# Optimization experiments

Hardware: AMD Instinct MI355X
Metric: run time of the kernel (lower is better)

Reference implementation:

```python
import jax, jax.numpy as jnp
import numpy as np

B = 128          # graphs
N = 512          # nodes per graph
NT = B * N       # total nodes = 65536
E = NT * 16      # total edges = 1048576
IN = 64
H = 128
OUT = 2
L = 4            # num_layers
RATIO = 0.8


def setup_inputs() -> dict:
    key = jax.random.key(0)
    ks = jax.random.split(key, 20)

    def w(k, shape, fan_in):
        return jax.random.normal(k, shape, jnp.float32) / np.sqrt(fan_in)

    x = jax.random.normal(ks[0], (NT, IN), jnp.float32)
    edge_index = jax.random.randint(ks[1], (2, E), 0, NT, dtype=jnp.int32)
    batch = (jnp.arange(NT) // N).astype(jnp.int32)  # equal-size graphs

    return {
        "x": x,
        "edge_index": edge_index,
        "batch": batch,
        # conv1: GraphConv(IN, H, aggr='mean') -> lin_rel (w/ bias) + lin_root (no bias)
        "W1_rel": w(ks[2], (IN, H), IN),
        "W1_root": w(ks[3], (IN, H), IN),
        "b1": jnp.zeros((H,), jnp.float32),
        # convs[0..2]: GraphConv(H, H, aggr='mean'), stacked
        "Wc_rel": w(ks[4], (L - 1, H, H), H),
        "Wc_root": w(ks[5], (L - 1, H, H), H),
        "bc": jnp.zeros((L - 1, H), jnp.float32),
        # SAGPooling score GNN: GraphConv(H, 1) with default aggr='add'
        "pw_rel": w(ks[6], (H,), H),
        "pw_root": w(ks[7], (H,), H),
        "pb": jnp.zeros((1,), jnp.float32),
        # MLP head
        "lin1_W": w(ks[8], (L * H, H), L * H),
        "lin1_b": jnp.zeros((H,), jnp.float32),
        "lin2_W": w(ks[9], (H, OUT), H),
        "lin2_b": jnp.zeros((OUT,), jnp.float32),
    }


def _graph_conv_mean(x, src, dst, emask, W_rel, W_root, b, n):
    # PyG GraphConv: lin_rel(mean_{j->i} x_j) + lin_root(x_i); masked edges excluded.
    msg = x[src] * emask[:, None]                                  # [E, D] gather
    s = jax.ops.segment_sum(msg, dst, num_segments=n)              # [n, D] scatter-add
    cnt = jax.ops.segment_sum(emask, dst, num_segments=n)          # [n]
    agg = s / jnp.maximum(cnt, 1.0)[:, None]                       # zero for isolated nodes
    return agg @ W_rel + x @ W_root + b


def reference(x, edge_index, batch, W1_rel, W1_root, b1, Wc_rel, Wc_root, bc,
              pw_rel, pw_root, pb, lin1_W, lin1_b, lin2_W, lin2_b):
    src = edge_index[0]
    dst = edge_index[1]
    emask = jnp.ones((E,), jnp.float32)
    n = NT
    npg = N  # nodes per graph (all graphs equal size)

    h = jax.nn.relu(_graph_conv_mean(x, src, dst, emask, W1_rel, W1_root, b1, n))
    xs = [h.reshape(B, npg, H).mean(axis=1)]  # global_mean_pool

    for i in range(L - 1):
        h = jax.nn.relu(_graph_conv_mean(h, src, dst, emask, Wc_rel[i], Wc_root[i], bc[i], n))
        xs.append(h.reshape(B, npg, H).mean(axis=1))
        if i % 2 == 0 and i < L - 2:
            # ---- SAGPooling: score via GraphConv(H,1) with add aggregation ----
            smsg = jax.ops.segment_sum(h[src] * emask[:, None], dst, num_segments=n)
            score = smsg @ pw_rel + h @ pw_root + pb[0]            # [n]
            k = int(np.ceil(RATIO * npg))
            topv, topi = jax.lax.top_k(score.reshape(B, npg), k)   # per-graph top-k
            perm = (jnp.arange(B)[:, None] * npg + topi).reshape(-1)  # global kept ids
            h = h[perm] * jnp.tanh(topv.reshape(-1))[:, None]
            # remap edges; edges touching dropped nodes get masked out
            node_map = jnp.full((n,), -1, jnp.int32).at[perm].set(
                jnp.arange(B * k, dtype=jnp.int32))
            ns, nd = node_map[src], node_map[dst]
            keep = ((ns >= 0) & (nd >= 0)).astype(jnp.float32)
            emask = emask * keep
            src = jnp.where(ns >= 0, ns, 0)
            dst = jnp.where(nd >= 0, nd, 0)
            n = B * k
            npg = k

    xcat = jnp.concatenate(xs, axis=-1)                            # JumpingKnowledge 'cat'
    out = jax.nn.relu(xcat @ lin1_W + lin1_b)
    # dropout is identity in eval mode
    out = out @ lin2_W + lin2_b
    return jax.nn.log_softmax(out, axis=-1)
```

## Files before the change

### kernel.cpp

```cpp
#include <hip/hip_runtime.h>
#include <math.h>

#define NT 65536
#define EE 1048576
#define NB 128
#define KK 410
#define HH 128

typedef short bf16x8 __attribute__((ext_vector_type(8)));
typedef float f32x4 __attribute__((ext_vector_type(4)));

__device__ unsigned short g_xb[(size_t)NT * 64];
__device__ unsigned short g_hb1[(size_t)NT * HH];
__device__ unsigned short g_hb2[(size_t)NT * HH];
__device__ unsigned short g_wt1[128 * 128];
__device__ unsigned short g_wtc[3 * 128 * 256];
__device__ unsigned short g_csr1u[EE];
__device__ unsigned short g_keptu[NT];
__device__ unsigned int g_ebuck[EE];
__device__ int g_bcnt[128];
__device__ int g_bcur[128];
__device__ float g_trel[NT];
__device__ float g_troot[NT];
__device__ float g_gatef[NT];
__device__ float g_kinv[NT];
__device__ float g_xc4[4 * NB * 4 * 128];
__device__ int g_rows1[NT + 1];

__device__ __forceinline__ unsigned short* ubuf(int id) {
    switch (id) {
        case 0: return g_xb;
        case 1: return g_hb1;
        case 2: return g_hb2;
        case 3: return g_wt1;
        case 4: return g_wtc;
    }
    return g_xb;
}

__device__ __forceinline__ float b2f(unsigned short u) {
    union { unsigned int i; float f; } v;
    v.i = ((unsigned int)u) << 16;
    return v.f;
}
__device__ __forceinline__ unsigned short f2b(float f) {
    unsigned int x = __float_as_uint(f);
    unsigned int r = x + 0x7fffu + ((x >> 16) & 1u);
    return (unsigned short)(r >> 16);
}
__device__ __forceinline__ bf16x8 scale8(bf16x8 a, float g) {
    bf16x8 r;
#pragma unroll
    for (int i = 0; i < 8; i++) {
        unsigned short u = (unsigned short)a[i];
        r[i] = (short)f2b(b2f(u) * g);
    }
    return r;
}

__global__ __launch_bounds__(256) void k_prep(const float* __restrict__ x,
                                              const float* __restrict__ W1r,
                                              const float* __restrict__ W1o,
                                              const float* __restrict__ Wcr,
                                              const float* __restrict__ Wco,
                                              const int* __restrict__ dst) {
    if (blockIdx.x < 4544) {
        int tid = blockIdx.x * 256 + threadIdx.x;
        if (tid < 1048576) {
            float4 v = *(const float4*)&x[(size_t)tid * 4];
            unsigned int lo = (unsigned int)f2b(v.x) | ((unsigned int)f2b(v.y) << 16);
            unsigned int hi = (unsigned int)f2b(v.z) | ((unsigned int)f2b(v.w) << 16);
            *(uint2*)&g_xb[(size_t)tid * 4] = make_uint2(lo, hi);
        } else if (tid < 1048576 + 16384) {
            int r = tid - 1048576;
            int k = r & 127, n = r >> 7;
            float v = (k < 64) ? W1r[k * 128 + n] : W1o[(k - 64) * 128 + n];
            g_wt1[n * 128 + k] = f2b(v);
        } else {
            int r = tid - (1048576 + 16384);
            int l = r >> 15;
            int k = r & 255, n = (r >> 8) & 127;
            float v = (k < 128) ? Wcr[l * 16384 + k * 128 + n]
                                : Wco[l * 16384 + (k - 128) * 128 + n];
            g_wtc[l * 32768 + n * 256 + k] = f2b(v);
        }
    } else {
        __shared__ int h[128];
        if (threadIdx.x < 128) h[threadIdx.x] = 0;
        __syncthreads();
        int e0 = ((blockIdx.x - 4544) * 256 + threadIdx.x) * 4;
        int4 d = *(const int4*)&dst[e0];
        atomicAdd(&h[d.x >> 9], 1);
        atomicAdd(&h[d.y >> 9], 1);
        atomicAdd(&h[d.z >> 9], 1);
        atomicAdd(&h[d.w >> 9], 1);
        __syncthreads();
        if (threadIdx.x < 128 && h[threadIdx.x]) atomicAdd(&g_bcnt[threadIdx.x], h[threadIdx.x]);
    }
}

__global__ __launch_bounds__(256) void k_bscatter(const int* __restrict__ src,
                                                  const int* __restrict__ dst) {
    __shared__ int h[128];
    __shared__ int base[128];
    __shared__ int sc[128];
    __shared__ int vv[128];
    int t = threadIdx.x;
    if (t < 128) { vv[t] = g_bcnt[t]; sc[t] = vv[t]; h[t] = 0; }
    __syncthreads();
    for (int off = 1; off < 128; off <<= 1) {
        int u = (t >= off && t < 128) ? sc[t - off] : 0;
        __syncthreads();
        if (t < 128) sc[t] += u;
        __syncthreads();
    }
    int e0 = (blockIdx.x * 256 + t) * 4;
    int4 s = *(const int4*)&src[e0];
    int4 d = *(const int4*)&dst[e0];
    int b0 = d.x >> 9, b1 = d.y >> 9, b2 = d.z >> 9, b3 = d.w >> 9;
    atomicAdd(&h[b0], 1);
    atomicAdd(&h[b1], 1);
    atomicAdd(&h[b2], 1);
    atomicAdd(&h[b3], 1);
    __syncthreads();
    if (t < 128) {
        int c = h[t];
        base[t] = (sc[t] - vv[t]) + (c ? atomicAdd(&g_bcur[t], c) : 0);
        h[t] = 0;
    }
    __syncthreads();
    int r0 = atomicAdd(&h[b0], 1);
    g_ebuck[base[b0] + r0] = ((unsigned int)(d.x & 511) << 16) | (unsigned int)s.x;
    int r1 = atomicAdd(&h[b1], 1);
    g_ebuck[base[b1] + r1] = ((unsigned int)(d.y & 511) << 16) | (unsigned int)s.y;
    int r2 = atomicAdd(&h[b2], 1);
    g_ebuck[base[b2] + r2] = ((unsigned int)(d.z & 511) << 16) | (unsigned int)s.z;
    int r3 = atomicAdd(&h[b3], 1);
    g_ebuck[base[b3] + r3] = ((unsigned int)(d.w & 511) << 16) | (unsigned int)s.w;
}

__global__ __launch_bounds__(512) void k_bcsr() {
    __shared__ int hist[512];
    __shared__ int offs[512];
    __shared__ int cur[512];
    __shared__ int sc[128];
    int g = blockIdx.x, t = threadIdx.x;
    if (t < 128) sc[t] = g_bcnt[t];
    hist[t] = 0;
    cur[t] = 0;
    __syncthreads();
    for (int off = 1; off < 128; off <<= 1) {
        int u = (t >= off && t < 128) ? sc[t - off] : 0;
        __syncthreads();
        if (t < 128) sc[t] += u;
        __syncthreads();
    }
    int b0 = sc[g] - g_bcnt[g];
    int b1 = sc[g];
    for (int e = b0 + t; e < b1; e += 512) {
        unsigned int p = g_ebuck[e];
        atomicAdd(&hist[p >> 16], 1);
    }
    __syncthreads();
    int v = hist[t];
    offs[t] = v;
    __syncthreads();
    for (int off = 1; off < 512; off <<= 1) {
        int u = (t >= off) ? offs[t - off] : 0;
        __syncthreads();
        offs[t] += u;
        __syncthreads();
    }
    int excl = offs[t] - v;
    g_rows1[g * 512 + t] = b0 + excl;
    if (t == 511) g_rows1[g * 512 + 512] = b0 + excl + v;
    __syncthreads();
    offs[t] = excl;
    __syncthreads();
    for (int e = b0 + t; e < b1; e += 512) {
        unsigned int p = g_ebuck[e];
        int dl = p >> 16;
        int r = atomicAdd(&cur[dl], 1);
        g_csr1u[b0 + offs[dl] + r] = (unsigned short)(p & 0xFFFFu);
    }
}

template <int KA, int KB, int KC, int GATED, int MASKED, int DOTS, int BGATE>
__global__ __launch_bounds__(512) void k_conv(int hId, int bId, int wId, int wOfs,
                                              const float* __restrict__ bias, int outId,
                                              int sec,
                                              const float* __restrict__ pwr,
                                              const float* __restrict__ pwt) {
    constexpr int STR = KA + 8;
    __shared__ unsigned short lds_a[128 * STR];
    __shared__ float s[128];
    const unsigned short* h = ubuf(hId);
    const unsigned short* Bp = ubuf(bId);
    const unsigned short* Wt = ubuf(wId) + wOfs;
    unsigned short* out = ubuf(outId);
    int rowbase = blockIdx.x * 128;

    {
        constexpr int TPN = KA / 8;
        constexpr int RPP = 512 / TPN;
        int local = threadIdx.x / TPN;
        int t = threadIdx.x % TPN;
        const unsigned short* ht = h + t * 8;
#pragma unroll 1
        for (int pass = 0; pass < 128 / RPP; pass++) {
            int rl = pass * RPP + local;
            int node = rowbase + rl;
            int r0 = g_rows1[node], r1 = g_rows1[node + 1];
            float kinv_pre = (KC == 2) ? g_kinv[node] : 0.f;
            float acc[8];
#pragma unroll
            for (int i = 0; i < 8; i++) acc[i] = 0.f;
            int kc = 0;
#define ACCV(v, gf)                                              \
    acc[0] += gf * b2f((unsigned short)(v.x & 0xffff));          \
    acc[1] += gf * b2f((unsigned short)(v.x >> 16));             \
    acc[2] += gf * b2f((unsigned short)(v.y & 0xffff));          \
    acc[3] += gf * b2f((unsigned short)(v.y >> 16));             \
    acc[4] += gf * b2f((unsigned short)(v.z & 0xffff));          \
    acc[5] += gf * b2f((unsigned short)(v.z >> 16));             \
    acc[6] += gf * b2f((unsigned short)(v.w & 0xffff));          \
    acc[7] += gf * b2f((unsigned short)(v.w >> 16));
            int e = r0;
            for (; e + 4 <= r1; e += 4) {
                int i0 = g_csr1u[e], i1 = g_csr1u[e + 1];
                int i2 = g_csr1u[e + 2], i3 = g_csr1u[e + 3];
                uint4 v0 = *(const uint4*)&ht[(size_t)i0 * KA];
                uint4 v1 = *(const uint4*)&ht[(size_t)i1 * KA];
                uint4 v2 = *(const uint4*)&ht[(size_t)i2 * KA];
                uint4 v3 = *(const uint4*)&ht[(size_t)i3 * KA];
                float g0 = GATED ? g_gatef[i0] : 1.0f;
                float g1 = GATED ? g_gatef[i1] : 1.0f;
                float g2 = GATED ? g_gatef[i2] : 1.0f;
                float g3 = GATED ? g_gatef[i3] : 1.0f;
                if (KC == 1)
                    kc += (int)g_keptu[i0] + (int)g_keptu[i1]
                        + (int)g_keptu[i2] + (int)g_keptu[i3];
                ACCV(v0, g0) ACCV(v1, g1) ACCV(v2, g2) ACCV(v3, g3)
            }
            for (; e < r1; e++) {
                int i0 = g_csr1u[e];
                uint4 v0 = *(const uint4*)&ht[(size_t)i0 * KA];
                float g0 = GATED ? g_gatef[i0] : 1.0f;
                if (KC == 1) kc += (int)g_keptu[i0];
                ACCV(v0, g0)
            }
#undef ACCV
            float inv;
            if (KC == 0) {
                int c = r1 - r0;
                inv = 1.0f / (float)(c > 0 ? c : 1);
            } else if (KC == 1) {
                inv = 1.0f / (float)(kc > 0 ? kc : 1);
                if (t == 0) g_kinv[node] = inv;
            } else {
                inv = kinv_pre;
            }
            uint4 o;
            o.x = (unsigned int)f2b(acc[0] * inv) | ((unsigned int)f2b(acc[1] * inv) << 16);
            o.y = (unsigned int)f2b(acc[2] * inv) | ((unsigned int)f2b(acc[3] * inv) << 16);
            o.z = (unsigned int)f2b(acc[4] * inv) | ((unsigned int)f2b(acc[5] * inv) << 16);
            o.w = (unsigned int)f2b(acc[6] * inv) | ((unsigned int)f2b(acc[7] * inv) << 16);
            *(uint4*)&lds_a[rl * STR + t * 8] = o;
        }
    }
    __syncthreads();

    const int K = KA + KB;
    int lane = threadIdx.x & 63;
    int w = threadIdx.x >> 6;
    int n16 = lane & 15, quad = lane >> 4;
    int rowloc = w * 16;
    int rowg = rowbase + rowloc;
    int g = blockIdx.x >> 2, qb = blockIdx.x & 3;
    float ga0 = BGATE ? g_gatef[rowg + n16] : 1.0f;
    f32x4 acc[8];
#pragma unroll
    for (int ct = 0; ct < 8; ct++)
#pragma unroll
        for (int i = 0; i < 4; i++) acc[ct][i] = 0.f;

#pragma unroll
    for (int ks = 0; ks < K / 32; ks++) {
        int k0 = ks * 32;
        bf16x8 a0;
        if (k0 < KA) {
            a0 = *(const bf16x8*)&lds_a[(rowloc + n16) * STR + k0 + quad * 8];
        } else {
            int kk = k0 - KA;
            a0 = *(const bf16x8*)&Bp[(size_t)(rowg + n16) * KB + kk + quad * 8];
            if (BGATE) a0 = scale8(a0, ga0);
        }
#pragma unroll
        for (int ct = 0; ct < 8; ct++) {
            bf16x8 b = *(const bf16x8*)&Wt[(size_t)(ct * 16 + n16) * K + k0 + quad * 8];
            acc[ct] = __builtin_amdgcn_mfma_f32_16x16x32_bf16(a0, b, acc[ct], 0, 0, 0);
        }
    }

    if (threadIdx.x < 128) s[threadIdx.x] = 0.f;
    {
        float m[4];
#pragma unroll
        for (int i = 0; i < 4; i++) {
            int r = rowg + quad * 4 + i;
            m[i] = (!MASKED || g_keptu[r]) ? 1.0f : 0.0f;
        }
#pragma unroll
        for (int ct = 0; ct < 8; ct++) {
            int c = ct * 16 + n16;
            float bv = bias[c];
#pragma unroll
            for (int i = 0; i < 4; i++) {
                int r = rowg + quad * 4 + i;
                float v = fmaxf(acc[ct][i] + bv, 0.f) * m[i];
                acc[ct][i] = v;
                out[(size_t)r * 128 + c] = f2b(v);
            }
        }
    }
    __syncthreads();

#pragma unroll
    for (int ct = 0; ct < 8; ct++) {
        float p = acc[ct][0] + acc[ct][1] + acc[ct][2] + acc[ct][3];
        p += __shfl_xor(p, 16);
        p += __shfl_xor(p, 32);
        if (quad == 0) atomicAdd(&s[ct * 16 + n16], p);
    }

    if (DOTS) {
        float pr[8], pt[8];
#pragma unroll
        for (int ct = 0; ct < 8; ct++) {
            pr[ct] = pwr[ct * 16 + n16];
            pt[ct] = pwt[ct * 16 + n16];
        }
#pragma unroll
        for (int i = 0; i < 4; i++) {
            float dr = 0.f, dt = 0.f;
#pragma unroll
            for (int ct = 0; ct < 8; ct++) {
                dr += acc[ct][i] * pr[ct];
                dt += acc[ct][i] * pt[ct];
            }
            dr += __shfl_xor(dr, 1); dt += __shfl_xor(dt, 1);
            dr += __shfl_xor(dr, 2); dt += __shfl_xor(dt, 2);
            dr += __shfl_xor(dr, 4); dt += __shfl_xor(dt, 4);
            dr += __shfl_xor(dr, 8); dt += __shfl_xor(dt, 8);
            if (n16 == 0) {
                int r = rowg + quad * 4 + i;
                g_trel[r] = dr;
                g_troot[r] = dt;
            }
        }
    }
    __syncthreads();
    if (threadIdx.x < 128)
        g_xc4[((sec * NB + g) * 4 + qb) * 128 + threadIdx.x] = s[threadIdx.x];
}

__global__ __launch_bounds__(256) void k_topk(const float* __restrict__ pb) {
    __shared__ float sv[512];
    __shared__ int si[512];
    int g = blockIdx.x, t = threadIdx.x;
    if (t == 0) { g_bcnt[g] = 0; g_bcur[g] = 0; }
    float pbv = pb[0];
    for (int l = t; l < 512; l += 256) {
        int node = g * 512 + l;
        int r0 = g_rows1[node], r1 = g_rows1[node + 1];
        float s = 0.f;
        int e = r0;
        for (; e + 4 <= r1; e += 4) {
            float s0 = g_trel[g_csr1u[e]];
            float s1 = g_trel[g_csr1u[e + 1]];
            float s2 = g_trel[g_csr1u[e + 2]];
            float s3 = g_trel[g_csr1u[e + 3]];
            s += (s0 + s1) + (s2 + s3);
        }
        for (; e < r1; e++) s += g_trel[g_csr1u[e]];
        sv[l] = s + g_troot[node] + pbv;
        si[l] = l;
    }
    __syncthreads();
    for (int k = 2; k <= 512; k <<= 1) {
        for (int j = k >> 1; j > 0; j >>= 1) {
            for (int i = t; i < 512; i += 256) {
                int p = i ^ j;
                if (p > i) {
                    float va = sv[i], vb = sv[p];
                    int ia = si[i], ib = si[p];
                    bool aFirst = (va > vb) || (va == vb && ia < ib);
                    bool up = ((i & k) == 0);
                    if (up != aFirst) { sv[i] = vb; sv[p] = va; si[i] = ib; si[p] = ia; }
                }
            }
            __syncthreads();
        }
    }
    for (int r = t; r < 512; r += 256) {
        int old = g * 512 + si[r];
        if (r < KK) {
            g_gatef[old] = tanhf(sv[r]);
            g_keptu[old] = 1;
        } else {
            g_gatef[old] = 0.f;
            g_keptu[old] = 0;
        }
    }
}

__global__ __launch_bounds__(128) void k_head(const float* __restrict__ W1, const float* __restrict__ b1,
                                              const float* __restrict__ W2, const float* __restrict__ b2,
                                              float* __restrict__ out) {
    __shared__ float xr[512];
    __shared__ float r0[128], r1[128];
    int g = blockIdx.x, t = threadIdx.x;
    for (int i = t; i < 512; i += 128) {
        int sec = i >> 7, c = i & 127;
        const float* p = &g_xc4[((sec * NB + g) * 4) * 128 + c];
        float v = p[0] + p[128] + p[256] + p[384];
        float inv = (sec < 2) ? (1.0f / 512.0f) : (1.0f / 410.0f);
        xr[i] = v * inv;
    }
    __syncthreads();
    float acc = b1[t];
    for (int k = 0; k < 512; k++) acc += xr[k] * W1[k * 128 + t];
    acc = fmaxf(acc, 0.f);
    r0[t] = acc * W2[t * 2 + 0];
    r1[t] = acc * W2[t * 2 + 1];
    __syncthreads();
    for (int off = 64; off > 0; off >>= 1) {
        if (t < off) { r0[t] += r0[t + off]; r1[t] += r1[t + off]; }
        __syncthreads();
    }
    if (t == 0) {
        float z0 = r0[0] + b2[0], z1 = r1[0] + b2[1];
        float m = fmaxf(z0, z1);
        float l = m + logf(expf(z0 - m) + expf(z1 - m));
        out[g * 2 + 0] = z0 - l;
        out[g * 2 + 1] = z1 - l;
    }
}

extern "C" void kernel_launch(void* const* d_in, const int* in_sizes, int n_in,
                              void* d_out, int out_size, void* d_ws, size_t ws_size,
                              hipStream_t stream) {
    const float* x = (const float*)d_in[0];
    const int* ei = (const int*)d_in[1];
    const int* src = ei;
    const int* dst = ei + EE;
    const float* W1r = (const float*)d_in[3];
    const float* W1o = (const float*)d_in[4];
    const float* b1 = (const float*)d_in[5];
    const float* Wcr = (const float*)d_in[6];
    const float* Wco = (const float*)d_in[7];
    const float* bc = (const float*)d_in[8];
    const float* pwr = (const float*)d_in[9];
    const float* pwt = (const float*)d_in[10];
    const float* pb = (const float*)d_in[11];
    const float* l1W = (const float*)d_in[12];
    const float* l1b = (const float*)d_in[13];
    const float* l2W = (const float*)d_in[14];
    const float* l2b = (const float*)d_in[15];
    float* out = (float*)d_out;

    k_prep<<<5568, 256, 0, stream>>>(x, W1r, W1o, Wcr, Wco, dst);

    k_bscatter<<<1024, 256, 0, stream>>>(src, dst);
    k_bcsr<<<128, 512, 0, stream>>>();

    k_conv<64, 64, 0, 0, 0, 0, 0><<<512, 512, 0, stream>>>(0, 0, 3, 0, b1, 1, 0, pwr, pwt);

    k_conv<128, 128, 0, 0, 0, 1, 0><<<512, 512, 0, stream>>>(1, 1, 4, 0, bc, 2, 1, pwr, pwt);

    k_topk<<<NB, 256, 0, stream>>>(pb);

    k_conv<128, 128, 1, 1, 1, 0, 1><<<512, 512, 0, stream>>>(2, 2, 4, 32768, bc + 128, 1, 2, pwr, pwt);

    k_conv<128, 128, 2, 0, 1, 0, 0><<<512, 512, 0, stream>>>(1, 1, 4, 65536, bc + 256, 2, 3, pwr, pwt);

    k_head<<<NB, 128, 0, stream>>>(l1W, l1b, l2W, l2b, out);
}
```

Baseline: 500.8 us.

## Aggregate neighbors directly into MFMA A-fragments in registers, drop LDS staging

The conv kernel's gather-mean aggregation now has each lane accumulate the exact bf16x8 slice it will feed to the MFMA as its A operand. Aggregated rows therefore stay in registers instead of being written to LDS and read back after a barrier. Blocks shrink to 256 threads covering 64 rows, so the grid doubles and the pooled-sum partials buffer grows from 4 to 8 slots per graph, with the head summing 8. Each lane now issues 16 B gathers per channel chunk for its node, which raises register pressure and changes the memory-level parallelism of the gather.

```diff
diff --git a/kernel.cpp b/kernel.cpp
--- a/kernel.cpp
+++ b/kernel.cpp
@@ -24,7 +24,7 @@
 __device__ float g_troot[NT];
 __device__ float g_gatef[NT];
 __device__ float g_kinv[NT];
-__device__ float g_xc4[4 * NB * 4 * 128];
+__device__ float g_xc8[4 * NB * 8 * 128];
 __device__ int g_rows1[NT + 1];
 
 __device__ __forceinline__ unsigned short* ubuf(int id) {
@@ -186,123 +186,114 @@
 }
 
 template <int KA, int KB, int KC, int GATED, int MASKED, int DOTS, int BGATE>
-__global__ __launch_bounds__(512) void k_conv(int hId, int bId, int wId, int wOfs,
-                                              const float* __restrict__ bias, int outId,
-                                              int sec,
-                                              const float* __restrict__ pwr,
-                                              const float* __restrict__ pwt) {
-    constexpr int STR = KA + 8;
-    __shared__ unsigned short lds_a[128 * STR];
-    __shared__ float s[128];
+__global__ __launch_bounds__(256, 4) void k_conv(int hId, int bId, int wId, int wOfs,
+                                                 const float* __restrict__ bias, int outId,
+                                                 int sec,
+                                                 const float* __restrict__ pwr,
+                                                 const float* __restrict__ pwt) {
+    constexpr int NCHA = KA / 32;
+    const int K = KA + KB;
     const unsigned short* h = ubuf(hId);
     const unsigned short* Bp = ubuf(bId);
     const unsigned short* Wt = ubuf(wId) + wOfs;
     unsigned short* out = ubuf(outId);
-    int rowbase = blockIdx.x * 128;
-
-    {
-        constexpr int TPN = KA / 8;
-        constexpr int RPP = 512 / TPN;
-        int local = threadIdx.x / TPN;
-        int t = threadIdx.x % TPN;
-        const unsigned short* ht = h + t * 8;
-#pragma unroll 1
-        for (int pass = 0; pass < 128 / RPP; pass++) {
-            int rl = pass * RPP + local;
-            int node = rowbase + rl;
-            int r0 = g_rows1[node], r1 = g_rows1[node + 1];
-            float kinv_pre = (KC == 2) ? g_kinv[node] : 0.f;
-            float acc[8];
-#pragma unroll
-            for (int i = 0; i < 8; i++) acc[i] = 0.f;
-            int kc = 0;
-#define ACCV(v, gf)                                              \
-    acc[0] += gf * b2f((unsigned short)(v.x & 0xffff));          \
-    acc[1] += gf * b2f((unsigned short)(v.x >> 16));             \
-    acc[2] += gf * b2f((unsigned short)(v.y & 0xffff));          \
-    acc[3] += gf * b2f((unsigned short)(v.y >> 16));             \
-    acc[4] += gf * b2f((unsigned short)(v.z & 0xffff));          \
-    acc[5] += gf * b2f((unsigned short)(v.z >> 16));             \
-    acc[6] += gf * b2f((unsigned short)(v.w & 0xffff));          \
-    acc[7] += gf * b2f((unsigned short)(v.w >> 16));
-            int e = r0;
-            for (; e + 4 <= r1; e += 4) {
-                int i0 = g_csr1u[e], i1 = g_csr1u[e + 1];
-                int i2 = g_csr1u[e + 2], i3 = g_csr1u[e + 3];
-                uint4 v0 = *(const uint4*)&ht[(size_t)i0 * KA];
-                uint4 v1 = *(const uint4*)&ht[(size_t)i1 * KA];
-                uint4 v2 = *(const uint4*)&ht[(size_t)i2 * KA];
-                uint4 v3 = *(const uint4*)&ht[(size_t)i3 * KA];
-                float g0 = GATED ? g_gatef[i0] : 1.0f;
-                float g1 = GATED ? g_gatef[i1] : 1.0f;
-                float g2 = GATED ? g_gatef[i2] : 1.0f;
-                float g3 = GATED ? g_gatef[i3] : 1.0f;
-                if (KC == 1)
-                    kc += (int)g_keptu[i0] + (int)g_keptu[i1]
-                        + (int)g_keptu[i2] + (int)g_keptu[i3];
-                ACCV(v0, g0) ACCV(v1, g1) ACCV(v2, g2) ACCV(v3, g3)
-            }
-            for (; e < r1; e++) {
-                int i0 = g_csr1u[e];
-                uint4 v0 = *(const uint4*)&ht[(size_t)i0 * KA];
-                float g0 = GATED ? g_gatef[i0] : 1.0f;
-                if (KC == 1) kc += (int)g_keptu[i0];
-                ACCV(v0, g0)
-            }
-#undef ACCV
-            float inv;
-            if (KC == 0) {
-                int c = r1 - r0;
-                inv = 1.0f / (float)(c > 0 ? c : 1);
-            } else if (KC == 1) {
-                inv = 1.0f / (float)(kc > 0 ? kc : 1);
-                if (t == 0) g_kinv[node] = inv;
-            } else {
-                inv = kinv_pre;
-            }
-            uint4 o;
-            o.x = (unsigned int)f2b(acc[0] * inv) | ((unsigned int)f2b(acc[1] * inv) << 16);
-            o.y = (unsigned int)f2b(acc[2] * inv) | ((unsigned int)f2b(acc[3] * inv) << 16);
-            o.z = (unsigned int)f2b(acc[4] * inv) | ((unsigned int)f2b(acc[5] * inv) << 16);
-            o.w = (unsigned int)f2b(acc[6] * inv) | ((unsigned int)f2b(acc[7] * inv) << 16);
-            *(uint4*)&lds_a[rl * STR + t * 8] = o;
-        }
-    }
-    __syncthreads();
-
-    const int K = KA + KB;
+    __shared__ float s[128];
     int lane = threadIdx.x & 63;
     int w = threadIdx.x >> 6;
     int n16 = lane & 15, quad = lane >> 4;
-    int rowloc = w * 16;
-    int rowg = rowbase + rowloc;
-    int g = blockIdx.x >> 2, qb = blockIdx.x & 3;
-    float ga0 = BGATE ? g_gatef[rowg + n16] : 1.0f;
+    int rowbase = blockIdx.x * 64;
+    int rowg = rowbase + w * 16;
+    int node = rowg + n16;
+    if (threadIdx.x < 128) s[threadIdx.x] = 0.f;
+
+    int r0 = g_rows1[node], r1 = g_rows1[node + 1];
+    float aggacc[NCHA][8];
+#pragma unroll
+    for (int ch = 0; ch < NCHA; ch++)
+#pragma unroll
+        for (int j = 0; j < 8; j++) aggacc[ch][j] = 0.f;
+    int kc = 0;
+    const unsigned short* hq = h + quad * 8;
+#define ACC8(arow, v, gf)                                        \
+    arow[0] += gf * b2f((unsigned short)(v.x & 0xffff));         \
+    arow[1] += gf * b2f((unsigned short)(v.x >> 16));            \
+    arow[2] += gf * b2f((unsigned short)(v.y & 0xffff));         \
+    arow[3] += gf * b2f((unsigned short)(v.y >> 16));            \
+    arow[4] += gf * b2f((unsigned short)(v.z & 0xffff));         \
+    arow[5] += gf * b2f((unsigned short)(v.z >> 16));            \
+    arow[6] += gf * b2f((unsigned short)(v.w & 0xffff));         \
+    arow[7] += gf * b2f((unsigned short)(v.w >> 16));
+    int e = r0;
+    for (; e + 2 <= r1; e += 2) {
+        int i0 = g_csr1u[e], i1 = g_csr1u[e + 1];
+        uint4 v0[NCHA], v1[NCHA];
+#pragma unroll
+        for (int ch = 0; ch < NCHA; ch++)
+            v0[ch] = *(const uint4*)&hq[(size_t)i0 * KA + ch * 32];
+#pragma unroll
+        for (int ch = 0; ch < NCHA; ch++)
+            v1[ch] = *(const uint4*)&hq[(size_t)i1 * KA + ch * 32];
+        float gf0 = GATED ? g_gatef[i0] : 1.0f;
+        float gf1 = GATED ? g_gatef[i1] : 1.0f;
+        if (KC == 1) kc += (int)g_keptu[i0] + (int)g_keptu[i1];
+#pragma unroll
+        for (int ch = 0; ch < NCHA; ch++) { ACC8(aggacc[ch], v0[ch], gf0) }
+#pragma unroll
+        for (int ch = 0; ch < NCHA; ch++) { ACC8(aggacc[ch], v1[ch], gf1) }
+    }
+    if (e < r1) {
+        int i0 = g_csr1u[e];
+        uint4 v0[NCHA];
+#pragma unroll
+        for (int ch = 0; ch < NCHA; ch++)
+            v0[ch] = *(const uint4*)&hq[(size_t)i0 * KA + ch * 32];
+        float gf0 = GATED ? g_gatef[i0] : 1.0f;
+        if (KC == 1) kc += (int)g_keptu[i0];
+#pragma unroll
+        for (int ch = 0; ch < NCHA; ch++) { ACC8(aggacc[ch], v0[ch], gf0) }
+    }
+#undef ACC8
+    float inv;
+    if (KC == 0) {
+        int c = r1 - r0;
+        inv = 1.0f / (float)(c > 0 ? c : 1);
+    } else if (KC == 1) {
+        inv = 1.0f / (float)(kc > 0 ? kc : 1);
+        if (quad == 0) g_kinv[node] = inv;
+    } else {
+        inv = g_kinv[node];
+    }
+
+    bf16x8 afrag[NCHA];
+#pragma unroll
+    for (int ch = 0; ch < NCHA; ch++)
+#pragma unroll
+        for (int j = 0; j < 8; j++) afrag[ch][j] = (short)f2b(aggacc[ch][j] * inv);
+
+    float ga = BGATE ? g_gatef[node] : 1.0f;
     f32x4 acc[8];
 #pragma unroll
     for (int ct = 0; ct < 8; ct++)
 #pragma unroll
         for (int i = 0; i < 4; i++) acc[ct][i] = 0.f;
-
-#pragma unroll
-    for (int ks = 0; ks < K / 32; ks++) {
-        int k0 = ks * 32;
-        bf16x8 a0;
-        if (k0 < KA) {
-            a0 = *(const bf16x8*)&lds_a[(rowloc + n16) * STR + k0 + quad * 8];
+#pragma unroll
+    for (int ks = 0; ks < 8; ks++) {
+        if (ks >= K / 32) break;
+        bf16x8 a;
+        if (ks < NCHA) {
+            a = afrag[ks];
         } else {
-            int kk = k0 - KA;
-            a0 = *(const bf16x8*)&Bp[(size_t)(rowg + n16) * KB + kk + quad * 8];
-            if (BGATE) a0 = scale8(a0, ga0);
+            int kk = (ks - NCHA) * 32;
+            a = *(const bf16x8*)&Bp[(size_t)node * KB + kk + quad * 8];
+            if (BGATE) a = scale8(a, ga);
         }
 #pragma unroll
         for (int ct = 0; ct < 8; ct++) {
-            bf16x8 b = *(const bf16x8*)&Wt[(size_t)(ct * 16 + n16) * K + k0 + quad * 8];
-            acc[ct] = __builtin_amdgcn_mfma_f32_16x16x32_bf16(a0, b, acc[ct], 0, 0, 0);
-        }
-    }
-
-    if (threadIdx.x < 128) s[threadIdx.x] = 0.f;
+            bf16x8 b = *(const bf16x8*)&Wt[(size_t)(ct * 16 + n16) * K + ks * 32 + quad * 8];
+            acc[ct] = __builtin_amdgcn_mfma_f32_16x16x32_bf16(a, b, acc[ct], 0, 0, 0);
+        }
+    }
+
     {
         float m[4];
 #pragma unroll
@@ -360,8 +351,10 @@
         }
     }
     __syncthreads();
-    if (threadIdx.x < 128)
-        g_xc4[((sec * NB + g) * 4 + qb) * 128 + threadIdx.x] = s[threadIdx.x];
+    if (threadIdx.x < 128) {
+        int g = blockIdx.x >> 3, e8 = blockIdx.x & 7;
+        g_xc8[((sec * NB + g) * 8 + e8) * 128 + threadIdx.x] = s[threadIdx.x];
+    }
 }
 
 __global__ __launch_bounds__(256) void k_topk(const float* __restrict__ pb) {
@@ -422,8 +415,10 @@
     int g = blockIdx.x, t = threadIdx.x;
     for (int i = t; i < 512; i += 128) {
         int sec = i >> 7, c = i & 127;
-        const float* p = &g_xc4[((sec * NB + g) * 4) * 128 + c];
-        float v = p[0] + p[128] + p[256] + p[384];
+        const float* p = &g_xc8[((sec * NB + g) * 8) * 128 + c];
+        float v = 0.f;
+#pragma unroll
+        for (int q = 0; q < 8; q++) v += p[q * 128];
         float inv = (sec < 2) ? (1.0f / 512.0f) : (1.0f / 410.0f);
         xr[i] = v * inv;
     }
@@ -474,15 +469,15 @@
     k_bscatter<<<1024, 256, 0, stream>>>(src, dst);
     k_bcsr<<<128, 512, 0, stream>>>();
 
-    k_conv<64, 64, 0, 0, 0, 0, 0><<<512, 512, 0, stream>>>(0, 0, 3, 0, b1, 1, 0, pwr, pwt);
-
-    k_conv<128, 128, 0, 0, 0, 1, 0><<<512, 512, 0, stream>>>(1, 1, 4, 0, bc, 2, 1, pwr, pwt);
+    k_conv<64, 64, 0, 0, 0, 0, 0><<<1024, 256, 0, stream>>>(0, 0, 3, 0, b1, 1, 0, pwr, pwt);
+
+    k_conv<128, 128, 0, 0, 0, 1, 0><<<1024, 256, 0, stream>>>(1, 1, 4, 0, bc, 2, 1, pwr, pwt);
 
     k_topk<<<NB, 256, 0, stream>>>(pb);
 
-    k_conv<128, 128, 1, 1, 1, 0, 1><<<512, 512, 0, stream>>>(2, 2, 4, 32768, bc + 128, 1, 2, pwr, pwt);
-
-    k_conv<128, 128, 2, 0, 1, 0, 0><<<512, 512, 0, stream>>>(1, 1, 4, 65536, bc + 256, 2, 3, pwr, pwt);
+    k_conv<128, 128, 1, 1, 1, 0, 1><<<1024, 256, 0, stream>>>(2, 2, 4, 32768, bc + 128, 1, 2, pwr, pwt);
+
+    k_conv<128, 128, 2, 0, 1, 0, 0><<<1024, 256, 0, stream>>>(1, 1, 4, 65536, bc + 256, 2, 3, pwr, pwt);
 
     k_head<<<NB, 128, 0, stream>>>(l1W, l1b, l2W, l2b, out);
 }
```

After: 511.4 us. +2.1%, slower.
